# Optimization experiments

Hardware: AMD Instinct MI355X
Metric: run time of the kernel (lower is better)

The kernel has to match this reference:

```python
import jax, jax.numpy as jnp
import numpy as np

NC = 30      # n_centres in HyperNetwork RBFs
WIDTH = 64
D = 32
BATCH = 1048576


def _rbf_linear(t, centres, log_sigmas, lin_w, lin_b):
    # RBF_CNF(in_features=1) followed by nn.Linear; gaussian basis exp(-d^2)
    d = jnp.abs(t - centres[:, 0]) / jnp.exp(log_sigmas)   # (NC,) via broadcast of t (1,)
    phi = jnp.exp(-d * d)
    return phi @ lin_w.T + lin_b                            # (out_features,)


def setup_inputs() -> dict:
    key = jax.random.key(0)
    blocksize = WIDTH * D
    ks = jax.random.split(key, 10)

    def lin(k, out_f, in_f):
        bound = 1.0 / np.sqrt(in_f).astype(np.float32)
        kw, kb = jax.random.split(k)
        w = jax.random.uniform(kw, (out_f, in_f), jnp.float32, -bound, bound)
        b = jax.random.uniform(kb, (out_f,), jnp.float32, -bound, bound)
        return w, b

    W_lin_w, W_lin_b = lin(ks[0], blocksize, NC)
    U_lin_w, U_lin_b = lin(ks[1], blocksize, NC)
    B_lin_w, B_lin_b = lin(ks[2], WIDTH, NC)
    return dict(
        t=jax.random.uniform(ks[3], (1,), jnp.float32),
        z=jax.random.normal(ks[4], (BATCH, D), jnp.float32),
        logp_z=jnp.zeros((BATCH, 1), jnp.float32),
        W_centres=jax.random.normal(ks[5], (NC, 1), jnp.float32),
        W_log_sigmas=jnp.zeros((NC,), jnp.float32),
        W_lin_w=W_lin_w, W_lin_b=W_lin_b,
        U_centres=jax.random.normal(ks[6], (NC, 1), jnp.float32),
        U_log_sigmas=jnp.zeros((NC,), jnp.float32),
        U_lin_w=U_lin_w, U_lin_b=U_lin_b,
        B_centres=jax.random.normal(ks[7], (NC, 1), jnp.float32),
        B_log_sigmas=jnp.zeros((NC,), jnp.float32),
        B_lin_w=B_lin_w, B_lin_b=B_lin_b,
    )


def reference(t, z, logp_z,
              W_centres, W_log_sigmas, W_lin_w, W_lin_b,
              U_centres, U_log_sigmas, U_lin_w, U_lin_b,
              B_centres, B_log_sigmas, B_lin_w, B_lin_b):
    # Hypernetwork-generated weights at time t
    Wt = _rbf_linear(t, W_centres, W_log_sigmas, W_lin_w, W_lin_b).reshape(WIDTH, D)
    Ut = _rbf_linear(t, U_centres, U_log_sigmas, U_lin_w, U_lin_b).reshape(WIDTH, D)
    Bt = _rbf_linear(t, B_centres, B_log_sigmas, B_lin_w, B_lin_b)  # (WIDTH,)

    # h[w,b] = tanh(z_b . Wt_w + Bt_w); torch builds (WIDTH,B,D) copies, we fuse
    h = jnp.tanh(z @ Wt.T + Bt)        # (B, WIDTH)
    dz_dt = (h @ Ut) / WIDTH           # mean over width -> (B, D)

    # Exact Jacobian trace (what trace_df_dz computes via an autograd loop):
    # d dz_dt[b,i] / d z[b,i] = mean_w (1 - h[b,w]^2) * Wt[w,i] * Ut[w,i]
    wu = jnp.sum(Wt * Ut, axis=1)                 # (WIDTH,)
    trace = ((1.0 - h * h) @ wu) / WIDTH          # (B,)
    dlogp_z_dt = -trace[:, None]                  # (B, 1)
    return dz_dt, dlogp_z_dt
```

## Files before the change

kernel.cpp:

```cpp
#include <hip/hip_runtime.h>
#include <hip/hip_bf16.h>

#define NC 30
#define WIDTH 64
#define DD 32
#define BATCH_N 1048576

typedef __bf16 bf16x8 __attribute__((ext_vector_type(8)));
typedef float f32x4 __attribute__((ext_vector_type(4)));

__device__ __forceinline__ bf16x8 pack_bf8(float4 a, float4 b) {
    bf16x8 r;
    r[0] = (__bf16)a.x; r[1] = (__bf16)a.y; r[2] = (__bf16)a.z; r[3] = (__bf16)a.w;
    r[4] = (__bf16)b.x; r[5] = (__bf16)b.y; r[6] = (__bf16)b.z; r[7] = (__bf16)b.w;
    return r;
}

__global__ void hyper_rows(
    const float* __restrict__ t,
    const float* __restrict__ Wc, const float* __restrict__ Wls,
    const float* __restrict__ Ww, const float* __restrict__ Wb,
    const float* __restrict__ Uc, const float* __restrict__ Uls,
    const float* __restrict__ Uw, const float* __restrict__ Ub,
    const float* __restrict__ Bc, const float* __restrict__ Bls,
    const float* __restrict__ Bw, const float* __restrict__ Bb,
    float* __restrict__ outWt, float* __restrict__ outUtT,
    float* __restrict__ outBt, float* __restrict__ outwu)
{
    __shared__ float phiW[NC], phiU[NC], phiB[NC];
    const float tv = t[0];
    const int tid = threadIdx.x;
    if (tid < NC) {
        float dW = fabsf(tv - Wc[tid]) * __expf(-Wls[tid]);
        phiW[tid] = __expf(-dW * dW);
        float dU = fabsf(tv - Uc[tid]) * __expf(-Uls[tid]);
        phiU[tid] = __expf(-dU * dU);
        float dB = fabsf(tv - Bc[tid]) * __expf(-Bls[tid]);
        phiB[tid] = __expf(-dB * dB);
    }
    __syncthreads();
    const int j = blockIdx.x * blockDim.x + tid;
    float aw = Wb[j];
    float au = Ub[j];
    #pragma unroll
    for (int k = 0; k < NC; ++k) {
        aw += phiW[k] * Ww[j * NC + k];
        au += phiU[k] * Uw[j * NC + k];
    }
    outWt[j] = aw;
    const int w = j >> 5, i = j & 31;
    outUtT[i * WIDTH + w] = au;

    float p = aw * au;
    #pragma unroll
    for (int off = 1; off < 32; off <<= 1) p += __shfl_xor(p, off, 64);
    if ((tid & 31) == 0) outwu[w] = p;

    if (blockIdx.x == 0 && tid < WIDTH) {
        float ab = Bb[tid];
        #pragma unroll
        for (int k = 0; k < NC; ++k) ab += phiB[k] * Bw[tid * NC + k];
        outBt[tid] = ab;
    }
}

__global__ __launch_bounds__(256, 4) void cnf_main(
    const float* __restrict__ z,
    const float* __restrict__ Wt,
    const float* __restrict__ UtT,
    const float* __restrict__ Bt, const float* __restrict__ wu,
    float* __restrict__ dz, float* __restrict__ dlogp)
{
    __shared__ __bf16 hbuf[4][16][72];
    const int tid  = threadIdx.x;
    const int wave = tid >> 6;
    const int lane = tid & 63;
    const int l15  = lane & 15;
    const int quad = lane >> 4;
    __bf16 (*hl)[72] = hbuf[wave];

    bf16x8 bW[4];
    #pragma unroll
    for (int t4 = 0; t4 < 4; ++t4) {
        const float4* p = (const float4*)(Wt + (t4 * 16 + l15) * DD + quad * 8);
        bW[t4] = pack_bf8(p[0], p[1]);
    }
    bf16x8 bU[2][2];
    #pragma unroll
    for (int c = 0; c < 2; ++c)
        #pragma unroll
        for (int t2 = 0; t2 < 2; ++t2) {
            const float4* p = (const float4*)(UtT + (t2 * 16 + l15) * WIDTH + c * 32 + quad * 8);
            bU[c][t2] = pack_bf8(p[0], p[1]);
        }
    float bt_l[4], wu_l[4];
    #pragma unroll
    for (int t4 = 0; t4 < 4; ++t4) {
        bt_l[t4] = Bt[t4 * 16 + l15];
        wu_l[t4] = wu[t4 * 16 + l15];
    }

    const size_t gw = (size_t)blockIdx.x * 4 + wave;
    const float* zp = z + (gw * 128 + l15) * DD + quad * 8;

    float4 za = ((const float4*)zp)[0];
    float4 zb = ((const float4*)zp)[1];
    const f32x4 zero = {0.f, 0.f, 0.f, 0.f};
    const float inv = 1.0f / (float)WIDTH;

    for (int it = 0; it < 8; ++it) {
        float4 na = {0,0,0,0}, nb = {0,0,0,0};
        if (it < 7) {
            const float4* np = (const float4*)(zp + 16 * DD);
            na = np[0]; nb = np[1];
        }

        bf16x8 aZ = pack_bf8(za, zb);
        f32x4 accS[4];
        #pragma unroll
        for (int t4 = 0; t4 < 4; ++t4)
            accS[t4] = __builtin_amdgcn_mfma_f32_16x16x32_bf16(aZ, bW[t4], zero, 0, 0, 0);

        float part[4] = {0.f, 0.f, 0.f, 0.f};
        #pragma unroll
        for (int t4 = 0; t4 < 4; ++t4) {
            #pragma unroll
            for (int r = 0; r < 4; ++r) {
                const float s = accS[t4][r] + bt_l[t4];
                const float e = __expf(2.0f * s);
                const float h = 1.0f - 2.0f * __builtin_amdgcn_rcpf(e + 1.0f);
                part[r] += (1.0f - h * h) * wu_l[t4];
                hl[quad * 4 + r][t4 * 16 + l15] = (__bf16)h;
            }
        }

        bf16x8 aH0 = *(const bf16x8*)&hl[l15][quad * 8];
        bf16x8 aH1 = *(const bf16x8*)&hl[l15][32 + quad * 8];
        f32x4 accD[2];
        #pragma unroll
        for (int t2 = 0; t2 < 2; ++t2) {
            f32x4 c0 = __builtin_amdgcn_mfma_f32_16x16x32_bf16(aH0, bU[0][t2], zero, 0, 0, 0);
            accD[t2]  = __builtin_amdgcn_mfma_f32_16x16x32_bf16(aH1, bU[1][t2], c0, 0, 0, 0);
        }

        #pragma unroll
        for (int off = 1; off < 16; off <<= 1)
            #pragma unroll
            for (int r = 0; r < 4; ++r) part[r] += __shfl_xor(part[r], off, 64);

        const size_t row0 = gw * 128 + (size_t)it * 16 + quad * 4;
        if (l15 == 0) {
            #pragma unroll
            for (int r = 0; r < 4; ++r) dlogp[row0 + r] = -part[r] * inv;
        }

        #pragma unroll
        for (int t2 = 0; t2 < 2; ++t2)
            #pragma unroll
            for (int r = 0; r < 4; ++r)
                dz[(row0 + r) * DD + t2 * 16 + l15] = accD[t2][r] * inv;

        za = na; zb = nb;
        zp += 16 * DD;
    }
}

extern "C" void kernel_launch(void* const* d_in, const int* in_sizes, int n_in,
                              void* d_out, int out_size, void* d_ws, size_t ws_size,
                              hipStream_t stream)
{
    const float* t   = (const float*)d_in[0];
    const float* z   = (const float*)d_in[1];
    const float* Wc  = (const float*)d_in[3];
    const float* Wls = (const float*)d_in[4];
    const float* Ww  = (const float*)d_in[5];
    const float* Wb  = (const float*)d_in[6];
    const float* Uc  = (const float*)d_in[7];
    const float* Uls = (const float*)d_in[8];
    const float* Uw  = (const float*)d_in[9];
    const float* Ub  = (const float*)d_in[10];
    const float* Bc  = (const float*)d_in[11];
    const float* Bls = (const float*)d_in[12];
    const float* Bw  = (const float*)d_in[13];
    const float* Bb  = (const float*)d_in[14];

    float* wsWt  = (float*)d_ws;
    float* wsUtT = wsWt + 2048;
    float* wsBt  = wsUtT + 2048;
    float* wswu  = wsBt + 64;

    hyper_rows<<<16, 128, 0, stream>>>(t, Wc, Wls, Ww, Wb, Uc, Uls, Uw, Ub,
                                       Bc, Bls, Bw, Bb, wsWt, wsUtT, wsBt, wswu);

    float* dz = (float*)d_out;
    float* dlogp = dz + (size_t)BATCH_N * DD;
    cnf_main<<<2048, 256, 0, stream>>>(z, wsWt, wsUtT, wsBt, wswu, dz, dlogp);
}
```

Baseline: 281.8 us.

## Transpose first MFMA so tanh trace reduction shrinks and 1/WIDTH folds into hypernet

Swaps the operands of the first MFMA so each lane holds the hidden-width outputs of a single batch row. That makes the trace reduction a two-step cross-quad shuffle instead of a 16-lane butterfly over four partials, and lets h be written to shared memory as packed bf16x4 stores. The 1/WIDTH scale is folded into Ut and wu in the hypernetwork kernel, and tanh is rewritten with exp2 and fma using precomputed scaled biases. Each lane now keeps 32 bias/wu values in registers instead of 8, which raises register pressure.

```diff
diff --git a/kernel.cpp b/kernel.cpp
--- a/kernel.cpp
+++ b/kernel.cpp
@@ -7,6 +7,7 @@
 #define BATCH_N 1048576
 
 typedef __bf16 bf16x8 __attribute__((ext_vector_type(8)));
+typedef __bf16 bf16x4 __attribute__((ext_vector_type(4)));
 typedef float f32x4 __attribute__((ext_vector_type(4)));
 
 __device__ __forceinline__ bf16x8 pack_bf8(float4 a, float4 b) {
@@ -49,12 +50,12 @@
     }
     outWt[j] = aw;
     const int w = j >> 5, i = j & 31;
-    outUtT[i * WIDTH + w] = au;
+    outUtT[i * WIDTH + w] = au * 0.015625f;
 
     float p = aw * au;
     #pragma unroll
     for (int off = 1; off < 32; off <<= 1) p += __shfl_xor(p, off, 64);
-    if ((tid & 31) == 0) outwu[w] = p;
+    if ((tid & 31) == 0) outwu[w] = p * 0.015625f;
 
     if (blockIdx.x == 0 && tid < WIDTH) {
         float ab = Bb[tid];
@@ -93,12 +94,16 @@
             const float4* p = (const float4*)(UtT + (t2 * 16 + l15) * WIDTH + c * 32 + quad * 8);
             bU[c][t2] = pack_bf8(p[0], p[1]);
         }
-    float bt_l[4], wu_l[4];
-    #pragma unroll
-    for (int t4 = 0; t4 < 4; ++t4) {
-        bt_l[t4] = Bt[t4 * 16 + l15];
-        wu_l[t4] = wu[t4 * 16 + l15];
-    }
+    const float TWO_LOG2E = 2.8853900817779268f;
+    float bt2[16], wu4[16];
+    #pragma unroll
+    for (int t4 = 0; t4 < 4; ++t4)
+        #pragma unroll
+        for (int r = 0; r < 4; ++r) {
+            const int wdx = t4 * 16 + quad * 4 + r;
+            bt2[t4 * 4 + r] = TWO_LOG2E * Bt[wdx];
+            wu4[t4 * 4 + r] = 4.0f * wu[wdx];
+        }
 
     const size_t gw = (size_t)blockIdx.x * 4 + wave;
     const float* zp = z + (gw * 128 + l15) * DD + quad * 8;
@@ -106,7 +111,6 @@
     float4 za = ((const float4*)zp)[0];
     float4 zb = ((const float4*)zp)[1];
     const f32x4 zero = {0.f, 0.f, 0.f, 0.f};
-    const float inv = 1.0f / (float)WIDTH;
 
     for (int it = 0; it < 8; ++it) {
         float4 na = {0,0,0,0}, nb = {0,0,0,0};
@@ -119,19 +123,22 @@
         f32x4 accS[4];
         #pragma unroll
         for (int t4 = 0; t4 < 4; ++t4)
-            accS[t4] = __builtin_amdgcn_mfma_f32_16x16x32_bf16(aZ, bW[t4], zero, 0, 0, 0);
-
-        float part[4] = {0.f, 0.f, 0.f, 0.f};
+            accS[t4] = __builtin_amdgcn_mfma_f32_16x16x32_bf16(bW[t4], aZ, zero, 0, 0, 0);
+
+        float part = 0.f;
         #pragma unroll
         for (int t4 = 0; t4 < 4; ++t4) {
+            bf16x4 hp;
             #pragma unroll
             for (int r = 0; r < 4; ++r) {
-                const float s = accS[t4][r] + bt_l[t4];
-                const float e = __expf(2.0f * s);
-                const float h = 1.0f - 2.0f * __builtin_amdgcn_rcpf(e + 1.0f);
-                part[r] += (1.0f - h * h) * wu_l[t4];
-                hl[quad * 4 + r][t4 * 16 + l15] = (__bf16)h;
+                const float f = fmaf(accS[t4][r], TWO_LOG2E, bt2[t4 * 4 + r]);
+                const float e = exp2f(f);
+                const float u = __builtin_amdgcn_rcpf(e + 1.0f);
+                const float h = fmaf(-2.0f, u, 1.0f);
+                part = fmaf(fmaf(-u, u, u), wu4[t4 * 4 + r], part);
+                hp[r] = (__bf16)h;
             }
+            *(bf16x4*)(&hl[l15][t4 * 16 + quad * 4]) = hp;
         }
 
         bf16x8 aH0 = *(const bf16x8*)&hl[l15][quad * 8];
@@ -143,22 +150,17 @@
             accD[t2]  = __builtin_amdgcn_mfma_f32_16x16x32_bf16(aH1, bU[1][t2], c0, 0, 0, 0);
         }
 
-        #pragma unroll
-        for (int off = 1; off < 16; off <<= 1)
-            #pragma unroll
-            for (int r = 0; r < 4; ++r) part[r] += __shfl_xor(part[r], off, 64);
-
-        const size_t row0 = gw * 128 + (size_t)it * 16 + quad * 4;
-        if (l15 == 0) {
-            #pragma unroll
-            for (int r = 0; r < 4; ++r) dlogp[row0 + r] = -part[r] * inv;
-        }
+        part += __shfl_xor(part, 16, 64);
+        part += __shfl_xor(part, 32, 64);
+
+        const size_t row0 = gw * 128 + (size_t)it * 16;
+        if (quad == 0) dlogp[row0 + l15] = -part;
 
         #pragma unroll
         for (int t2 = 0; t2 < 2; ++t2)
             #pragma unroll
             for (int r = 0; r < 4; ++r)
-                dz[(row0 + r) * DD + t2 * 16 + l15] = accD[t2][r] * inv;
+                dz[(row0 + quad * 4 + r) * DD + t2 * 16 + l15] = accD[t2][r];
 
         za = na; zb = nb;
         zp += 16 * DD;
```

Result: no change. 282.1 us (+0.1%).
